# Performance work log

Measured on AMD Instinct MI355X. Metric: run time of the kernel, lower is better.

The kernel has to match this reference:

```python
import jax, jax.numpy as jnp
import numpy as np

H, C = 4, 32          # heads, out_channels
NEG_SLOPE = 0.2       # PyG GATConv default leaky-relu slope


def gat(x, edge_index, W, a_src, a_dst, b):
    """Single GATConv layer (concat heads, self-loops, no dropout).
    Returns output [N, H*C] and edge attention alpha [E+N, H]."""
    N = x.shape[0]
    h = (x @ W).reshape(N, H, C)                       # [N,H,C]
    loop = jnp.arange(N)
    src = jnp.concatenate([edge_index[0], loop])       # messages src -> dst
    dst = jnp.concatenate([edge_index[1], loop])
    a_s = jnp.sum(h * a_src, axis=-1)                  # [N,H]
    a_d = jnp.sum(h * a_dst, axis=-1)                  # [N,H]
    e = jax.nn.leaky_relu(a_s[src] + a_d[dst], NEG_SLOPE)   # [E+N,H]
    m = jax.ops.segment_max(e, dst, num_segments=N)
    p = jnp.exp(e - m[dst])
    z = jax.ops.segment_sum(p, dst, num_segments=N)
    alpha = p / z[dst]                                 # softmax per destination
    out = jax.ops.segment_sum(alpha[:, :, None] * h[src], dst, num_segments=N)
    return out.reshape(N, H * C) + b, alpha


def setup_inputs() -> dict:
    key = jax.random.key(0)
    ks = jax.random.split(key, 12)
    N, K, F_IN, E, Dg = 50000, 1000, 128, 800000, 8
    offsets = jnp.array([1, 2, 3, 5, 7, 11, 13, 17])   # circulant group graph

    x = jax.random.normal(ks[0], (N, F_IN), dtype=jnp.float32)
    edge_index = jax.random.randint(ks[1], (2, E), 0, N)
    x_g = jax.random.normal(ks[2], (K, F_IN), dtype=jnp.float32)

    src_g = jnp.repeat(jnp.arange(K), Dg)
    dst_g = (src_g + jnp.tile(offsets, K)) % K
    edge_index_g = jnp.stack([src_g, dst_g])           # [2, 8000]

    group_index = jax.random.randint(ks[3], (N,), 0, K)
    g = jnp.arange(K)[:, None]
    # symmetrized neighbor groups of each group (out- and in-neighbors), [K,16]
    nbr_idx = jnp.concatenate([(g + offsets) % K, (g - offsets) % K], axis=1)

    sc = 1.0 / np.sqrt(F_IN)
    sa = 1.0 / np.sqrt(C)
    return dict(
        x=x, edge_index=edge_index, x_g=x_g, edge_index_g=edge_index_g,
        group_index=group_index, nbr_idx=nbr_idx,
        W1=jax.random.normal(ks[4], (F_IN, H * C)) * sc,
        a_src1=jax.random.normal(ks[5], (H, C)) * sa,
        a_dst1=jax.random.normal(ks[6], (H, C)) * sa,
        b1=jnp.zeros((H * C,), jnp.float32),
        W2=jax.random.normal(ks[7], (F_IN, H * C)) * sc,
        a_src2=jax.random.normal(ks[8], (H, C)) * sa,
        a_dst2=jax.random.normal(ks[9], (H, C)) * sa,
        b2=jnp.zeros((H * C,), jnp.float32),
    )


def reference(x, edge_index, x_g, edge_index_g, group_index, nbr_idx,
              W1, a_src1, a_dst1, b1, W2, a_src2, a_dst2, b2):
    x_out, alpha1 = gat(x, edge_index, W1, a_src1, a_dst1, b1)        # [N,128]
    x_g_out, alpha2 = gat(x_g, edge_index_g, W2, a_src2, a_dst2, b2)  # [K,128]

    # per-node attention over (own group + adjacent groups in E2)
    own = x_g_out[group_index]                    # [N,F]
    cand = x_g_out[nbr_idx[group_index]]          # [N,16,F] irregular gather
    s_self = jnp.sum(x_out * own, axis=-1, keepdims=True)      # [N,1]
    s_nbr = jnp.einsum('nf,nkf->nk', x_out, cand)              # [N,16]
    w = jax.nn.softmax(jnp.concatenate([s_self, s_nbr], axis=1), axis=1)
    group_out = w[:, :1] * own + jnp.einsum('nk,nkf->nf', w[:, 1:], cand)

    x_final = x_out * 0.5 + group_out * 0.5
    return (x_final, x_g_out, alpha1, alpha2)
```

## Files before the change

kernel.cpp:

```cpp
#include <hip/hip_runtime.h>
#include <math.h>

#define NS 0.2f

__device__ __forceinline__ float lrelu(float v){ return fmaxf(v, NS * v); }
__device__ __forceinline__ float sel4(float a, float b, float c, float d, int h){
    float ab = (h & 1) ? b : a;
    float cd = (h & 1) ? d : c;
    return (h & 2) ? cd : ab;
}

__global__ __launch_bounds__(256, 4) void gemm_attn(
    const float* __restrict__ X, const float* __restrict__ W,
    const float* __restrict__ a_src, const float* __restrict__ a_dst,
    float* __restrict__ Hout, float* __restrict__ AS, float* __restrict__ AD,
    int nrows)
{
    __shared__ float Wl[64 * 128];
    int tid = threadIdx.x;
    int cg  = tid & 31;
    int rg  = tid >> 5;
    int row0 = blockIdx.x * 48 + rg * 6;

    const float* xp[6];
    int rowv[6];
    #pragma unroll
    for (int r = 0; r < 6; ++r){
        rowv[r] = row0 + r;
        int rc = min(rowv[r], nrows - 1);
        xp[r] = X + (size_t)rc * 128;
    }

    float4 acc[6] = {};
    for (int kp = 0; kp < 2; ++kp){
        __syncthreads();
        const float4* wsrc = (const float4*)(W + (size_t)kp * 64 * 128);
        for (int i = tid; i < 64 * 32; i += 256) ((float4*)Wl)[i] = wsrc[i];
        __syncthreads();
        #pragma unroll 2
        for (int k = 0; k < 64; k += 4){
            float4 xv[6];
            #pragma unroll
            for (int r = 0; r < 6; ++r)
                xv[r] = *(const float4*)(xp[r] + kp * 64 + k);
            #pragma unroll
            for (int KK = 0; KK < 4; ++KK){
                float4 wv = *(const float4*)&Wl[(k + KK) * 128 + cg * 4];
                #pragma unroll
                for (int r = 0; r < 6; ++r){
                    float xs = (KK == 0) ? xv[r].x : (KK == 1) ? xv[r].y
                             : (KK == 2) ? xv[r].z : xv[r].w;
                    acc[r].x = fmaf(xs, wv.x, acc[r].x);
                    acc[r].y = fmaf(xs, wv.y, acc[r].y);
                    acc[r].z = fmaf(xs, wv.z, acc[r].z);
                    acc[r].w = fmaf(xs, wv.w, acc[r].w);
                }
            }
        }
    }

    float4 as4 = *(const float4*)&a_src[cg * 4];
    float4 ad4 = *(const float4*)&a_dst[cg * 4];
    int head = cg >> 3;
    #pragma unroll
    for (int r = 0; r < 6; ++r){
        bool ok = rowv[r] < nrows;
        if (ok) *(float4*)&Hout[(size_t)rowv[r] * 128 + cg * 4] = acc[r];
        float s1 = acc[r].x * as4.x + acc[r].y * as4.y + acc[r].z * as4.z + acc[r].w * as4.w;
        float s2 = acc[r].x * ad4.x + acc[r].y * ad4.y + acc[r].z * ad4.z + acc[r].w * ad4.w;
        #pragma unroll
        for (int off = 1; off < 8; off <<= 1){
            s1 += __shfl_xor(s1, off);
            s2 += __shfl_xor(s2, off);
        }
        if (ok && (cg & 7) == 0){
            AS[(size_t)rowv[r] * 4 + head] = s1;
            AD[(size_t)rowv[r] * 4 + head] = s2;
        }
    }
}

__global__ void count_rank_k(
    const int* __restrict__ ei1, int E1, int N1, int* __restrict__ cnt1, int* __restrict__ rank1,
    const int* __restrict__ ei2, int E2, int N2, int* __restrict__ cnt2, int* __restrict__ rank2)
{
    int i = blockIdx.x * blockDim.x + threadIdx.x;
    int T1 = E1 + N1, T2 = E2 + N2;
    if (i < T1){
        int dst = (i < E1) ? ei1[E1 + i] : (i - E1);
        rank1[i] = atomicAdd(&cnt1[dst], 1);
    } else {
        int j = i - T1;
        if (j < T2){
            int dst = (j < E2) ? ei2[E2 + j] : (j - E2);
            rank2[j] = atomicAdd(&cnt2[dst], 1);
        }
    }
}

__global__ void fill_k(
    const int* __restrict__ ei1, int E1, int N1, const int* __restrict__ rp1,
    const int* __restrict__ rank1, int* __restrict__ cs1, int* __restrict__ ce1,
    const int* __restrict__ ei2, int E2, int N2, const int* __restrict__ rp2,
    const int* __restrict__ rank2, int* __restrict__ cs2, int* __restrict__ ce2)
{
    int i = blockIdx.x * blockDim.x + threadIdx.x;
    int T1 = E1 + N1, T2 = E2 + N2;
    if (i < T1){
        int src, dst;
        if (i < E1){ src = ei1[i]; dst = ei1[E1 + i]; } else { src = dst = i - E1; }
        int pos = rp1[dst] + rank1[i];
        cs1[pos] = src;
        ce1[pos] = i;
    } else {
        int j = i - T1;
        if (j < T2){
            int src, dst;
            if (j < E2){ src = ei2[j]; dst = ei2[E2 + j]; } else { src = dst = j - E2; }
            int pos = rp2[dst] + rank2[j];
            cs2[pos] = src;
            ce2[pos] = j;
        }
    }
}

__global__ __launch_bounds__(1024) void scan_k(
    const int* __restrict__ c1, int n1, int* __restrict__ rp1,
    const int* __restrict__ c2, int n2, int* __restrict__ rp2)
{
    const int* counts = blockIdx.x ? c2 : c1;
    int n             = blockIdx.x ? n2 : n1;
    int* row_ptr      = blockIdx.x ? rp2 : rp1;

    __shared__ int wpart[16];
    __shared__ int carry_lds;
    int tid = threadIdx.x, lane = tid & 63, wid = tid >> 6;
    if (tid == 0) carry_lds = 0;
    __syncthreads();
    for (int base = 0; base < n; base += 8192){
        int idx = base + tid * 8;
        int v[8];
        #pragma unroll
        for (int j = 0; j < 8; ++j){
            int i = idx + j;
            v[j] = (i < n) ? counts[i] : 0;
        }
        int run[8]; int tot = 0;
        #pragma unroll
        for (int j = 0; j < 8; ++j){ run[j] = tot; tot += v[j]; }
        int x = tot;
        #pragma unroll
        for (int off = 1; off < 64; off <<= 1){
            int y = __shfl_up(x, off);
            if (lane >= off) x += y;
        }
        if (lane == 63) wpart[wid] = x;
        __syncthreads();
        if (tid < 16){
            int w = wpart[tid];
            #pragma unroll
            for (int off = 1; off < 16; off <<= 1){
                int y = __shfl_up(w, off);
                if (tid >= off) w += y;
            }
            wpart[tid] = w;
        }
        __syncthreads();
        int carry = carry_lds;
        int thr_excl = carry + (wid ? wpart[wid - 1] : 0) + x - tot;
        #pragma unroll
        for (int j = 0; j < 8; ++j){
            int i = idx + j;
            if (i < n) row_ptr[i] = thr_excl + run[j];
        }
        __syncthreads();
        if (tid == 0) carry_lds += wpart[15];
        __syncthreads();
    }
    if (tid == 0) row_ptr[n] = carry_lds;
}

__global__ __launch_bounds__(256) void aggregate(
    const int* __restrict__ row_ptr, const int* __restrict__ csr_src,
    const int* __restrict__ csr_eid, const float* __restrict__ Hbuf,
    const float* __restrict__ AS, const float* __restrict__ AD,
    const float* __restrict__ bias,
    float* __restrict__ alpha_out, float* __restrict__ out, int ndst)
{
    int gw = (int)((blockIdx.x * (size_t)blockDim.x + threadIdx.x) >> 6);
    if (gw >= ndst) return;
    int lane = threadIdx.x & 63;
    int s = row_ptr[gw], e = row_ptr[gw + 1];
    const float4 ad4 = *(const float4*)&AD[(size_t)gw * 4];

    int i0 = s + lane;
    bool has = (i0 < e);
    int src0 = 0, eid0 = 0;
    float4 e4 = make_float4(-INFINITY, -INFINITY, -INFINITY, -INFINITY);
    if (has){
        src0 = csr_src[i0];
        eid0 = csr_eid[i0];
        float4 a = *(const float4*)&AS[(size_t)src0 * 4];
        e4.x = lrelu(a.x + ad4.x); e4.y = lrelu(a.y + ad4.y);
        e4.z = lrelu(a.z + ad4.z); e4.w = lrelu(a.w + ad4.w);
    }
    float m0 = e4.x, m1 = e4.y, m2 = e4.z, m3 = e4.w;
    for (int i = s + 64 + lane; i < e; i += 64){
        int src = csr_src[i];
        float4 a = *(const float4*)&AS[(size_t)src * 4];
        m0 = fmaxf(m0, lrelu(a.x + ad4.x)); m1 = fmaxf(m1, lrelu(a.y + ad4.y));
        m2 = fmaxf(m2, lrelu(a.z + ad4.z)); m3 = fmaxf(m3, lrelu(a.w + ad4.w));
    }
    #pragma unroll
    for (int off = 32; off >= 1; off >>= 1){
        m0 = fmaxf(m0, __shfl_xor(m0, off));
        m1 = fmaxf(m1, __shfl_xor(m1, off));
        m2 = fmaxf(m2, __shfl_xor(m2, off));
        m3 = fmaxf(m3, __shfl_xor(m3, off));
    }
    float4 p4 = make_float4(0.f, 0.f, 0.f, 0.f);
    if (has){
        p4.x = __expf(e4.x - m0); p4.y = __expf(e4.y - m1);
        p4.z = __expf(e4.z - m2); p4.w = __expf(e4.w - m3);
    }
    float z0 = p4.x, z1 = p4.y, z2 = p4.z, z3 = p4.w;
    for (int i = s + 64 + lane; i < e; i += 64){
        int src = csr_src[i];
        float4 a = *(const float4*)&AS[(size_t)src * 4];
        z0 += __expf(lrelu(a.x + ad4.x) - m0);
        z1 += __expf(lrelu(a.y + ad4.y) - m1);
        z2 += __expf(lrelu(a.z + ad4.z) - m2);
        z3 += __expf(lrelu(a.w + ad4.w) - m3);
    }
    #pragma unroll
    for (int off = 32; off >= 1; off >>= 1){
        z0 += __shfl_xor(z0, off);
        z1 += __shfl_xor(z1, off);
        z2 += __shfl_xor(z2, off);
        z3 += __shfl_xor(z3, off);
    }
    float4 rz = make_float4(1.f / z0, 1.f / z1, 1.f / z2, 1.f / z3);

    if (has){
        float4 al;
        al.x = p4.x * rz.x; al.y = p4.y * rz.y;
        al.z = p4.z * rz.z; al.w = p4.w * rz.w;
        *(float4*)&alpha_out[(size_t)eid0 * 4] = al;
    }
    for (int i = s + 64 + lane; i < e; i += 64){
        int src = csr_src[i]; int eid = csr_eid[i];
        float4 a = *(const float4*)&AS[(size_t)src * 4];
        float4 al;
        al.x = __expf(lrelu(a.x + ad4.x) - m0) * rz.x;
        al.y = __expf(lrelu(a.y + ad4.y) - m1) * rz.y;
        al.z = __expf(lrelu(a.z + ad4.z) - m2) * rz.z;
        al.w = __expf(lrelu(a.w + ad4.w) - m3) * rz.w;
        *(float4*)&alpha_out[(size_t)eid * 4] = al;
    }

    int sub = lane >> 5, c = lane & 31, head = c >> 3;
    float mh  = sel4(m0, m1, m2, m3, head);
    float rzh = sel4(rz.x, rz.y, rz.z, rz.w, head);
    float adh = sel4(ad4.x, ad4.y, ad4.z, ad4.w, head);
    float4 acc0 = make_float4(0.f, 0.f, 0.f, 0.f);
    float4 acc1 = make_float4(0.f, 0.f, 0.f, 0.f);
    int ne   = e - s;
    int nreg = min(ne, 64);
    int nit  = (nreg + 3) >> 2;
    for (int j = 0; j < nit; ++j){
        int idx0 = 4 * j + sub;
        int idx1 = idx0 + 2;
        bool v0 = idx0 < nreg, v1 = idx1 < nreg;
        int r0 = v0 ? idx0 : 0, r1 = v1 ? idx1 : 0;
        float ax0 = __shfl(p4.x, r0), ay0 = __shfl(p4.y, r0);
        float az0 = __shfl(p4.z, r0), aw0 = __shfl(p4.w, r0);
        int sv0 = __shfl(src0, r0);
        float ax1 = __shfl(p4.x, r1), ay1 = __shfl(p4.y, r1);
        float az1 = __shfl(p4.z, r1), aw1 = __shfl(p4.w, r1);
        int sv1 = __shfl(src0, r1);
        float ph0 = v0 ? sel4(ax0, ay0, az0, aw0, head) : 0.f;
        float ph1 = v1 ? sel4(ax1, ay1, az1, aw1, head) : 0.f;
        const float4 hv0 = *(const float4*)&Hbuf[(size_t)sv0 * 128 + c * 4];
        const float4 hv1 = *(const float4*)&Hbuf[(size_t)sv1 * 128 + c * 4];
        acc0.x = fmaf(ph0, hv0.x, acc0.x);
        acc0.y = fmaf(ph0, hv0.y, acc0.y);
        acc0.z = fmaf(ph0, hv0.z, acc0.z);
        acc0.w = fmaf(ph0, hv0.w, acc0.w);
        acc1.x = fmaf(ph1, hv1.x, acc1.x);
        acc1.y = fmaf(ph1, hv1.y, acc1.y);
        acc1.z = fmaf(ph1, hv1.z, acc1.z);
        acc1.w = fmaf(ph1, hv1.w, acc1.w);
    }
    for (int t = s + 64 + sub; t < e; t += 2){
        int srcv = csr_src[t];
        float a = AS[(size_t)srcv * 4 + head];
        float ph = __expf(lrelu(a + adh) - mh);
        const float4 hv = *(const float4*)&Hbuf[(size_t)srcv * 128 + c * 4];
        acc0.x = fmaf(ph, hv.x, acc0.x);
        acc0.y = fmaf(ph, hv.y, acc0.y);
        acc0.z = fmaf(ph, hv.z, acc0.z);
        acc0.w = fmaf(ph, hv.w, acc0.w);
    }
    float4 acc;
    acc.x = acc0.x + acc1.x;
    acc.y = acc0.y + acc1.y;
    acc.z = acc0.z + acc1.z;
    acc.w = acc0.w + acc1.w;
    acc.x += __shfl_xor(acc.x, 32);
    acc.y += __shfl_xor(acc.y, 32);
    acc.z += __shfl_xor(acc.z, 32);
    acc.w += __shfl_xor(acc.w, 32);
    if (sub == 0){
        float4 bv = *(const float4*)&bias[c * 4];
        float4 o;
        o.x = acc.x * rzh + bv.x;
        o.y = acc.y * rzh + bv.y;
        o.z = acc.z * rzh + bv.z;
        o.w = acc.w * rzh + bv.w;
        *(float4*)&out[(size_t)gw * 128 + c * 4] = o;
    }
}

__global__ __launch_bounds__(256) void mix_k(
    const int* __restrict__ group_index, const int* __restrict__ nbr_idx,
    const float* __restrict__ xg, float* __restrict__ xf, int N)
{
    int gwv = (int)((blockIdx.x * (size_t)blockDim.x + threadIdx.x) >> 6);
    int lane = threadIdx.x & 63;
    int sl = lane & 15, ns = lane >> 4;
    int gw = gwv * 4 + ns;
    bool valid = gw < N;
    int gwc = min(gw, N - 1);
    int g = group_index[gwc];
    int ch = sl * 8;

    const float* xfrow = xf + (size_t)gwc * 128 + ch;
    float4 xa = *(const float4*)xfrow;
    float4 xb = *(const float4*)(xfrow + 4);

    int ids[17];
    ids[0] = g;
    {
        const int4* nb = (const int4*)&nbr_idx[g * 16];
        int4 n0 = nb[0], n1 = nb[1], n2 = nb[2], n3 = nb[3];
        ids[1] = n0.x;  ids[2] = n0.y;  ids[3] = n0.z;  ids[4] = n0.w;
        ids[5] = n1.x;  ids[6] = n1.y;  ids[7] = n1.z;  ids[8] = n1.w;
        ids[9] = n2.x;  ids[10] = n2.y; ids[11] = n2.z; ids[12] = n2.w;
        ids[13] = n3.x; ids[14] = n3.y; ids[15] = n3.z; ids[16] = n3.w;
    }

    float dn[17];
    #pragma unroll
    for (int k = 0; k < 17; ++k){
        const float* cr = xg + (size_t)ids[k] * 128 + ch;
        float4 ca = *(const float4*)cr;
        float4 cb = *(const float4*)(cr + 4);
        float d = xa.x * ca.x + xa.y * ca.y + xa.z * ca.z + xa.w * ca.w
                + xb.x * cb.x + xb.y * cb.y + xb.z * cb.z + xb.w * cb.w;
        d += __shfl_xor(d, 1);
        d += __shfl_xor(d, 2);
        d += __shfl_xor(d, 4);
        d += __shfl_xor(d, 8);
        dn[k] = d;
    }

    float mx = dn[0];
    #pragma unroll
    for (int k = 1; k < 17; ++k) mx = fmaxf(mx, dn[k]);
    float w[17]; float sum = 0.f;
    #pragma unroll
    for (int k = 0; k < 17; ++k){ w[k] = __expf(dn[k] - mx); sum += w[k]; }
    float inv = 1.0f / sum;

    float4 aa = make_float4(0.f, 0.f, 0.f, 0.f);
    float4 ab = make_float4(0.f, 0.f, 0.f, 0.f);
    #pragma unroll
    for (int k = 0; k < 17; ++k){
        const float* cr = xg + (size_t)ids[k] * 128 + ch;
        float4 ca = *(const float4*)cr;
        float4 cb = *(const float4*)(cr + 4);
        aa.x = fmaf(w[k], ca.x, aa.x); aa.y = fmaf(w[k], ca.y, aa.y);
        aa.z = fmaf(w[k], ca.z, aa.z); aa.w = fmaf(w[k], ca.w, aa.w);
        ab.x = fmaf(w[k], cb.x, ab.x); ab.y = fmaf(w[k], cb.y, ab.y);
        ab.z = fmaf(w[k], cb.z, ab.z); ab.w = fmaf(w[k], cb.w, ab.w);
    }

    if (valid){
        float* orow = xf + (size_t)gw * 128 + ch;
        float4 r0, r1;
        r0.x = 0.5f * xa.x + 0.5f * aa.x * inv;
        r0.y = 0.5f * xa.y + 0.5f * aa.y * inv;
        r0.z = 0.5f * xa.z + 0.5f * aa.z * inv;
        r0.w = 0.5f * xa.w + 0.5f * aa.w * inv;
        r1.x = 0.5f * xb.x + 0.5f * ab.x * inv;
        r1.y = 0.5f * xb.y + 0.5f * ab.y * inv;
        r1.z = 0.5f * xb.z + 0.5f * ab.z * inv;
        r1.w = 0.5f * xb.w + 0.5f * ab.w * inv;
        *(float4*)orow = r0;
        *(float4*)(orow + 4) = r1;
    }
}

extern "C" void kernel_launch(void* const* d_in, const int* in_sizes, int n_in,
                              void* d_out, int out_size, void* d_ws, size_t ws_size,
                              hipStream_t stream)
{
    const float* x    = (const float*)d_in[0];
    const int*   ei   = (const int*)  d_in[1];
    const float* xg   = (const float*)d_in[2];
    const int*   eig  = (const int*)  d_in[3];
    const int*   gidx = (const int*)  d_in[4];
    const int*   nbr  = (const int*)  d_in[5];
    const float* W1   = (const float*)d_in[6];
    const float* as1w = (const float*)d_in[7];
    const float* ad1w = (const float*)d_in[8];
    const float* b1   = (const float*)d_in[9];
    const float* W2   = (const float*)d_in[10];
    const float* as2w = (const float*)d_in[11];
    const float* ad2w = (const float*)d_in[12];
    const float* b2   = (const float*)d_in[13];

    const int N  = in_sizes[0] / 128;
    const int E  = in_sizes[1] / 2;
    const int K  = in_sizes[2] / 128;
    const int Eg = in_sizes[3] / 2;
    const int ET1 = E + N;
    const int ET2 = Eg + K;

    float* h1  = (float*)d_ws;
    float* h2  = h1 + (size_t)N * 128;
    float* as1 = h2 + (size_t)K * 128;
    float* ad1 = as1 + (size_t)N * 4;
    float* as2 = ad1 + (size_t)N * 4;
    float* ad2 = as2 + (size_t)K * 4;
    int* row_ptr1 = (int*)(ad2 + (size_t)K * 4);
    int* row_ptr2 = row_ptr1 + (N + 1);
    int* cnt1     = row_ptr2 + (K + 1);
    int* cnt2     = cnt1 + N;
    int* csr_src1 = cnt2 + K;
    int* csr_eid1 = csr_src1 + ET1;
    int* csr_src2 = csr_eid1 + ET1;
    int* csr_eid2 = csr_src2 + ET2;

    float* xfinal = (float*)d_out;
    float* xgout  = xfinal + (size_t)N * 128;
    float* alpha1 = xgout + (size_t)K * 128;
    float* alpha2 = alpha1 + (size_t)ET1 * 4;

    int* rank1 = (int*)alpha1;
    int* rank2 = (int*)alpha2;

    hipMemsetAsync(cnt1, 0, (size_t)(N + K) * sizeof(int), stream);

    int TT = ET1 + ET2;
    count_rank_k<<<(TT + 255) / 256, 256, 0, stream>>>(
        ei, E, N, cnt1, rank1, eig, Eg, K, cnt2, rank2);

    scan_k<<<2, 1024, 0, stream>>>(cnt1, N, row_ptr1, cnt2, K, row_ptr2);

    fill_k<<<(TT + 255) / 256, 256, 0, stream>>>(
        ei, E, N, row_ptr1, rank1, csr_src1, csr_eid1,
        eig, Eg, K, row_ptr2, rank2, csr_src2, csr_eid2);

    gemm_attn<<<(N + 47) / 48, 256, 0, stream>>>(x,  W1, as1w, ad1w, h1, as1, ad1, N);
    gemm_attn<<<(K + 47) / 48, 256, 0, stream>>>(xg, W2, as2w, ad2w, h2, as2, ad2, K);

    aggregate<<<(int)(((size_t)N * 64 + 255) / 256), 256, 0, stream>>>(
        row_ptr1, csr_src1, csr_eid1, h1, as1, ad1, b1, alpha1, xfinal, N);
    aggregate<<<(int)(((size_t)K * 64 + 255) / 256), 256, 0, stream>>>(
        row_ptr2, csr_src2, csr_eid2, h2, as2, ad2, b2, alpha2, xgout, K);

    mix_k<<<(int)(((size_t)N * 16 + 255) / 256), 256, 0, stream>>>(gidx, nbr, xgout, xfinal, N);
}
```

Measured before the change: 399.8 us.

## Store projected features in fp16 and fuse group mixing into node aggregation

The projected feature buffer H is now stored as half precision, which halves the bytes moved by the irregular per-edge gathers in aggregate. The group graph is computed first, and the final group-attention mix is folded into the node aggregate kernel's epilogue. This removes the separate mix_k pass that re-read and re-wrote the N x 128 output. The aggregate loop is simplified to recompute exp per edge instead of reusing register-cached probabilities via shuffles. This adds exp work and fp16 rounding error in the aggregated outputs.

```diff
diff --git a/kernel.cpp b/kernel.cpp
--- a/kernel.cpp
+++ b/kernel.cpp
@@ -1,5 +1,7 @@
 #include <hip/hip_runtime.h>
+#include <hip/hip_fp16.h>
 #include <math.h>
+#include <string.h>
 
 #define NS 0.2f
 
@@ -13,7 +15,7 @@
 __global__ __launch_bounds__(256, 4) void gemm_attn(
     const float* __restrict__ X, const float* __restrict__ W,
     const float* __restrict__ a_src, const float* __restrict__ a_dst,
-    float* __restrict__ Hout, float* __restrict__ AS, float* __restrict__ AD,
+    __half* __restrict__ Hout, float* __restrict__ AS, float* __restrict__ AD,
     int nrows)
 {
     __shared__ float Wl[64 * 128];
@@ -65,7 +67,13 @@
     #pragma unroll
     for (int r = 0; r < 6; ++r){
         bool ok = rowv[r] < nrows;
-        if (ok) *(float4*)&Hout[(size_t)rowv[r] * 128 + cg * 4] = acc[r];
+        if (ok){
+            __half2 p01 = __floats2half2_rn(acc[r].x, acc[r].y);
+            __half2 p23 = __floats2half2_rn(acc[r].z, acc[r].w);
+            __half2* hp = (__half2*)(Hout + (size_t)rowv[r] * 128 + cg * 4);
+            hp[0] = p01;
+            hp[1] = p23;
+        }
         float s1 = acc[r].x * as4.x + acc[r].y * as4.y + acc[r].z * as4.z + acc[r].w * as4.w;
         float s2 = acc[r].x * ad4.x + acc[r].y * ad4.y + acc[r].z * ad4.z + acc[r].w * ad4.w;
         #pragma unroll
@@ -180,12 +188,15 @@
     if (tid == 0) row_ptr[n] = carry_lds;
 }
 
+template<int GROUP>
 __global__ __launch_bounds__(256) void aggregate(
     const int* __restrict__ row_ptr, const int* __restrict__ csr_src,
-    const int* __restrict__ csr_eid, const float* __restrict__ Hbuf,
+    const int* __restrict__ csr_eid, const __half* __restrict__ Hbuf,
     const float* __restrict__ AS, const float* __restrict__ AD,
     const float* __restrict__ bias,
-    float* __restrict__ alpha_out, float* __restrict__ out, int ndst)
+    float* __restrict__ alpha_out, float* __restrict__ out, int ndst,
+    const int* __restrict__ group_index, const int* __restrict__ nbr_idx,
+    const float* __restrict__ xg)
 {
     int gw = (int)((blockIdx.x * (size_t)blockDim.x + threadIdx.x) >> 6);
     if (gw >= ndst) return;
@@ -262,142 +273,93 @@
     float mh  = sel4(m0, m1, m2, m3, head);
     float rzh = sel4(rz.x, rz.y, rz.z, rz.w, head);
     float adh = sel4(ad4.x, ad4.y, ad4.z, ad4.w, head);
-    float4 acc0 = make_float4(0.f, 0.f, 0.f, 0.f);
-    float4 acc1 = make_float4(0.f, 0.f, 0.f, 0.f);
-    int ne   = e - s;
-    int nreg = min(ne, 64);
-    int nit  = (nreg + 3) >> 2;
-    for (int j = 0; j < nit; ++j){
-        int idx0 = 4 * j + sub;
-        int idx1 = idx0 + 2;
-        bool v0 = idx0 < nreg, v1 = idx1 < nreg;
-        int r0 = v0 ? idx0 : 0, r1 = v1 ? idx1 : 0;
-        float ax0 = __shfl(p4.x, r0), ay0 = __shfl(p4.y, r0);
-        float az0 = __shfl(p4.z, r0), aw0 = __shfl(p4.w, r0);
-        int sv0 = __shfl(src0, r0);
-        float ax1 = __shfl(p4.x, r1), ay1 = __shfl(p4.y, r1);
-        float az1 = __shfl(p4.z, r1), aw1 = __shfl(p4.w, r1);
-        int sv1 = __shfl(src0, r1);
-        float ph0 = v0 ? sel4(ax0, ay0, az0, aw0, head) : 0.f;
-        float ph1 = v1 ? sel4(ax1, ay1, az1, aw1, head) : 0.f;
-        const float4 hv0 = *(const float4*)&Hbuf[(size_t)sv0 * 128 + c * 4];
-        const float4 hv1 = *(const float4*)&Hbuf[(size_t)sv1 * 128 + c * 4];
-        acc0.x = fmaf(ph0, hv0.x, acc0.x);
-        acc0.y = fmaf(ph0, hv0.y, acc0.y);
-        acc0.z = fmaf(ph0, hv0.z, acc0.z);
-        acc0.w = fmaf(ph0, hv0.w, acc0.w);
-        acc1.x = fmaf(ph1, hv1.x, acc1.x);
-        acc1.y = fmaf(ph1, hv1.y, acc1.y);
-        acc1.z = fmaf(ph1, hv1.z, acc1.z);
-        acc1.w = fmaf(ph1, hv1.w, acc1.w);
-    }
-    for (int t = s + 64 + sub; t < e; t += 2){
-        int srcv = csr_src[t];
-        float a = AS[(size_t)srcv * 4 + head];
-        float ph = __expf(lrelu(a + adh) - mh);
-        const float4 hv = *(const float4*)&Hbuf[(size_t)srcv * 128 + c * 4];
-        acc0.x = fmaf(ph, hv.x, acc0.x);
-        acc0.y = fmaf(ph, hv.y, acc0.y);
-        acc0.z = fmaf(ph, hv.z, acc0.z);
-        acc0.w = fmaf(ph, hv.w, acc0.w);
-    }
-    float4 acc;
-    acc.x = acc0.x + acc1.x;
-    acc.y = acc0.y + acc1.y;
-    acc.z = acc0.z + acc1.z;
-    acc.w = acc0.w + acc1.w;
+    float4 acc = make_float4(0.f, 0.f, 0.f, 0.f);
+    for (int t0 = s + sub; t0 < e; t0 += 4){
+        int t1 = t0 + 2;
+        bool v1 = t1 < e;
+        int u1 = v1 ? t1 : t0;
+        int sv0 = csr_src[t0];
+        int sv1 = csr_src[u1];
+        float a0 = AS[(size_t)sv0 * 4 + head];
+        float a1 = AS[(size_t)sv1 * 4 + head];
+        uint2 r0 = *(const uint2*)(Hbuf + (size_t)sv0 * 128 + c * 4);
+        uint2 r1 = *(const uint2*)(Hbuf + (size_t)sv1 * 128 + c * 4);
+        float ph0 = __expf(lrelu(a0 + adh) - mh);
+        float ph1 = v1 ? __expf(lrelu(a1 + adh) - mh) : 0.f;
+        __half2 h01, h23;
+        memcpy(&h01, &r0.x, 4); memcpy(&h23, &r0.y, 4);
+        float2 f01 = __half22float2(h01), f23 = __half22float2(h23);
+        acc.x = fmaf(ph0, f01.x, acc.x);
+        acc.y = fmaf(ph0, f01.y, acc.y);
+        acc.z = fmaf(ph0, f23.x, acc.z);
+        acc.w = fmaf(ph0, f23.y, acc.w);
+        memcpy(&h01, &r1.x, 4); memcpy(&h23, &r1.y, 4);
+        f01 = __half22float2(h01); f23 = __half22float2(h23);
+        acc.x = fmaf(ph1, f01.x, acc.x);
+        acc.y = fmaf(ph1, f01.y, acc.y);
+        acc.z = fmaf(ph1, f23.x, acc.z);
+        acc.w = fmaf(ph1, f23.y, acc.w);
+    }
     acc.x += __shfl_xor(acc.x, 32);
     acc.y += __shfl_xor(acc.y, 32);
     acc.z += __shfl_xor(acc.z, 32);
     acc.w += __shfl_xor(acc.w, 32);
+
+    float4 bv = *(const float4*)&bias[c * 4];
+    float4 o;
+    o.x = acc.x * rzh + bv.x;
+    o.y = acc.y * rzh + bv.y;
+    o.z = acc.z * rzh + bv.z;
+    o.w = acc.w * rzh + bv.w;
+
+    if (GROUP == 0){
+        if (sub == 0)
+            *(float4*)&out[(size_t)gw * 128 + c * 4] = o;
+        return;
+    }
+
     if (sub == 0){
-        float4 bv = *(const float4*)&bias[c * 4];
-        float4 o;
-        o.x = acc.x * rzh + bv.x;
-        o.y = acc.y * rzh + bv.y;
-        o.z = acc.z * rzh + bv.z;
-        o.w = acc.w * rzh + bv.w;
-        *(float4*)&out[(size_t)gw * 128 + c * 4] = o;
-    }
-}
-
-__global__ __launch_bounds__(256) void mix_k(
-    const int* __restrict__ group_index, const int* __restrict__ nbr_idx,
-    const float* __restrict__ xg, float* __restrict__ xf, int N)
-{
-    int gwv = (int)((blockIdx.x * (size_t)blockDim.x + threadIdx.x) >> 6);
-    int lane = threadIdx.x & 63;
-    int sl = lane & 15, ns = lane >> 4;
-    int gw = gwv * 4 + ns;
-    bool valid = gw < N;
-    int gwc = min(gw, N - 1);
-    int g = group_index[gwc];
-    int ch = sl * 8;
-
-    const float* xfrow = xf + (size_t)gwc * 128 + ch;
-    float4 xa = *(const float4*)xfrow;
-    float4 xb = *(const float4*)(xfrow + 4);
-
-    int ids[17];
-    ids[0] = g;
-    {
-        const int4* nb = (const int4*)&nbr_idx[g * 16];
-        int4 n0 = nb[0], n1 = nb[1], n2 = nb[2], n3 = nb[3];
-        ids[1] = n0.x;  ids[2] = n0.y;  ids[3] = n0.z;  ids[4] = n0.w;
-        ids[5] = n1.x;  ids[6] = n1.y;  ids[7] = n1.z;  ids[8] = n1.w;
-        ids[9] = n2.x;  ids[10] = n2.y; ids[11] = n2.z; ids[12] = n2.w;
-        ids[13] = n3.x; ids[14] = n3.y; ids[15] = n3.z; ids[16] = n3.w;
-    }
-
-    float dn[17];
-    #pragma unroll
-    for (int k = 0; k < 17; ++k){
-        const float* cr = xg + (size_t)ids[k] * 128 + ch;
-        float4 ca = *(const float4*)cr;
-        float4 cb = *(const float4*)(cr + 4);
-        float d = xa.x * ca.x + xa.y * ca.y + xa.z * ca.z + xa.w * ca.w
-                + xb.x * cb.x + xb.y * cb.y + xb.z * cb.z + xb.w * cb.w;
-        d += __shfl_xor(d, 1);
-        d += __shfl_xor(d, 2);
-        d += __shfl_xor(d, 4);
-        d += __shfl_xor(d, 8);
-        dn[k] = d;
-    }
-
-    float mx = dn[0];
-    #pragma unroll
-    for (int k = 1; k < 17; ++k) mx = fmaxf(mx, dn[k]);
-    float w[17]; float sum = 0.f;
-    #pragma unroll
-    for (int k = 0; k < 17; ++k){ w[k] = __expf(dn[k] - mx); sum += w[k]; }
-    float inv = 1.0f / sum;
-
-    float4 aa = make_float4(0.f, 0.f, 0.f, 0.f);
-    float4 ab = make_float4(0.f, 0.f, 0.f, 0.f);
-    #pragma unroll
-    for (int k = 0; k < 17; ++k){
-        const float* cr = xg + (size_t)ids[k] * 128 + ch;
-        float4 ca = *(const float4*)cr;
-        float4 cb = *(const float4*)(cr + 4);
-        aa.x = fmaf(w[k], ca.x, aa.x); aa.y = fmaf(w[k], ca.y, aa.y);
-        aa.z = fmaf(w[k], ca.z, aa.z); aa.w = fmaf(w[k], ca.w, aa.w);
-        ab.x = fmaf(w[k], cb.x, ab.x); ab.y = fmaf(w[k], cb.y, ab.y);
-        ab.z = fmaf(w[k], cb.z, ab.z); ab.w = fmaf(w[k], cb.w, ab.w);
-    }
-
-    if (valid){
-        float* orow = xf + (size_t)gw * 128 + ch;
-        float4 r0, r1;
-        r0.x = 0.5f * xa.x + 0.5f * aa.x * inv;
-        r0.y = 0.5f * xa.y + 0.5f * aa.y * inv;
-        r0.z = 0.5f * xa.z + 0.5f * aa.z * inv;
-        r0.w = 0.5f * xa.w + 0.5f * aa.w * inv;
-        r1.x = 0.5f * xb.x + 0.5f * ab.x * inv;
-        r1.y = 0.5f * xb.y + 0.5f * ab.y * inv;
-        r1.z = 0.5f * xb.z + 0.5f * ab.z * inv;
-        r1.w = 0.5f * xb.w + 0.5f * ab.w * inv;
-        *(float4*)orow = r0;
-        *(float4*)(orow + 4) = r1;
+        int g = group_index[gw];
+        int ids[17];
+        ids[0] = g;
+        #pragma unroll
+        for (int k = 0; k < 16; ++k) ids[k + 1] = nbr_idx[g * 16 + k];
+
+        float dn[17];
+        #pragma unroll
+        for (int k = 0; k < 17; ++k){
+            const float4 cv = *(const float4*)&xg[(size_t)ids[k] * 128 + c * 4];
+            float d = o.x * cv.x + o.y * cv.y + o.z * cv.z + o.w * cv.w;
+            d += __shfl_xor(d, 1);
+            d += __shfl_xor(d, 2);
+            d += __shfl_xor(d, 4);
+            d += __shfl_xor(d, 8);
+            d += __shfl_xor(d, 16);
+            dn[k] = d;
+        }
+        float mx = dn[0];
+        #pragma unroll
+        for (int k = 1; k < 17; ++k) mx = fmaxf(mx, dn[k]);
+        float wgt[17]; float sum = 0.f;
+        #pragma unroll
+        for (int k = 0; k < 17; ++k){ wgt[k] = __expf(dn[k] - mx); sum += wgt[k]; }
+        float inv = 1.0f / sum;
+
+        float4 ga = make_float4(0.f, 0.f, 0.f, 0.f);
+        #pragma unroll
+        for (int k = 0; k < 17; ++k){
+            const float4 cv = *(const float4*)&xg[(size_t)ids[k] * 128 + c * 4];
+            ga.x = fmaf(wgt[k], cv.x, ga.x);
+            ga.y = fmaf(wgt[k], cv.y, ga.y);
+            ga.z = fmaf(wgt[k], cv.z, ga.z);
+            ga.w = fmaf(wgt[k], cv.w, ga.w);
+        }
+        float4 r;
+        r.x = 0.5f * o.x + 0.5f * ga.x * inv;
+        r.y = 0.5f * o.y + 0.5f * ga.y * inv;
+        r.z = 0.5f * o.z + 0.5f * ga.z * inv;
+        r.w = 0.5f * o.w + 0.5f * ga.w * inv;
+        *(float4*)&out[(size_t)gw * 128 + c * 4] = r;
     }
 }
 
@@ -427,12 +389,12 @@
     const int ET1 = E + N;
     const int ET2 = Eg + K;
 
-    float* h1  = (float*)d_ws;
-    float* h2  = h1 + (size_t)N * 128;
-    float* as1 = h2 + (size_t)K * 128;
-    float* ad1 = as1 + (size_t)N * 4;
-    float* as2 = ad1 + (size_t)N * 4;
-    float* ad2 = as2 + (size_t)K * 4;
+    __half* h1 = (__half*)d_ws;
+    __half* h2 = h1 + (size_t)N * 128;
+    float*  as1 = (float*)(h2 + (size_t)K * 128);
+    float*  ad1 = as1 + (size_t)N * 4;
+    float*  as2 = ad1 + (size_t)N * 4;
+    float*  ad2 = as2 + (size_t)K * 4;
     int* row_ptr1 = (int*)(ad2 + (size_t)K * 4);
     int* row_ptr2 = row_ptr1 + (N + 1);
     int* cnt1     = row_ptr2 + (K + 1);
@@ -462,13 +424,13 @@
         ei, E, N, row_ptr1, rank1, csr_src1, csr_eid1,
         eig, Eg, K, row_ptr2, rank2, csr_src2, csr_eid2);
 
-    gemm_attn<<<(N + 47) / 48, 256, 0, stream>>>(x,  W1, as1w, ad1w, h1, as1, ad1, N);
     gemm_attn<<<(K + 47) / 48, 256, 0, stream>>>(xg, W2, as2w, ad2w, h2, as2, ad2, K);
-
-    aggregate<<<(int)(((size_t)N * 64 + 255) / 256), 256, 0, stream>>>(
-        row_ptr1, csr_src1, csr_eid1, h1, as1, ad1, b1, alpha1, xfinal, N);
-    aggregate<<<(int)(((size_t)K * 64 + 255) / 256), 256, 0, stream>>>(
-        row_ptr2, csr_src2, csr_eid2, h2, as2, ad2, b2, alpha2, xgout, K);
-
-    mix_k<<<(int)(((size_t)N * 16 + 255) / 256), 256, 0, stream>>>(gidx, nbr, xgout, xfinal, N);
-}
+    aggregate<0><<<(int)(((size_t)K * 64 + 255) / 256), 256, 0, stream>>>(
+        row_ptr2, csr_src2, csr_eid2, h2, as2, ad2, b2, alpha2, xgout, K,
+        nullptr, nullptr, nullptr);
+
+    gemm_attn<<<(N + 47) / 48, 256, 0, stream>>>(x, W1, as1w, ad1w, h1, as1, ad1, N);
+    aggregate<1><<<(int)(((size_t)N * 64 + 255) / 256), 256, 0, stream>>>(
+        row_ptr1, csr_src1, csr_eid1, h1, as1, ad1, b1, alpha1, xfinal, N,
+        gidx, nbr, xgout);
+}
```

New measurement: 439.4 us. +9.9%, slower.

## Store projected features in fp16 and compute alpha in a separate edge-order pass

Applied to the files above, without the earlier changes.

The projected node features h are now written as fp16, which halves the bytes moved by the random-gather aggregation loop. The CSR edge-id array is removed. Aggregate now writes per-destination max and sum, and a new edge-ordered kernel recomputes alpha with coalesced writes instead of scattered ones. The scan also handles 16 elements per thread and the launches are reordered. This adds fp16 rounding error to the output and recomputes the attention logits in the extra pass.

```diff
diff --git a/kernel.cpp b/kernel.cpp
--- a/kernel.cpp
+++ b/kernel.cpp
@@ -1,5 +1,7 @@
 #include <hip/hip_runtime.h>
+#include <hip/hip_fp16.h>
 #include <math.h>
+#include <string.h>
 
 #define NS 0.2f
 
@@ -13,7 +15,7 @@
 __global__ __launch_bounds__(256, 4) void gemm_attn(
     const float* __restrict__ X, const float* __restrict__ W,
     const float* __restrict__ a_src, const float* __restrict__ a_dst,
-    float* __restrict__ Hout, float* __restrict__ AS, float* __restrict__ AD,
+    __half* __restrict__ Hout, float* __restrict__ AS, float* __restrict__ AD,
     int nrows)
 {
     __shared__ float Wl[64 * 128];
@@ -65,7 +67,13 @@
     #pragma unroll
     for (int r = 0; r < 6; ++r){
         bool ok = rowv[r] < nrows;
-        if (ok) *(float4*)&Hout[(size_t)rowv[r] * 128 + cg * 4] = acc[r];
+        if (ok){
+            __half2 p01 = __floats2half2_rn(acc[r].x, acc[r].y);
+            __half2 p23 = __floats2half2_rn(acc[r].z, acc[r].w);
+            __half2* hp = (__half2*)(Hout + (size_t)rowv[r] * 128 + cg * 4);
+            hp[0] = p01;
+            hp[1] = p23;
+        }
         float s1 = acc[r].x * as4.x + acc[r].y * as4.y + acc[r].z * as4.z + acc[r].w * as4.w;
         float s2 = acc[r].x * ad4.x + acc[r].y * ad4.y + acc[r].z * ad4.z + acc[r].w * ad4.w;
         #pragma unroll
@@ -100,26 +108,22 @@
 
 __global__ void fill_k(
     const int* __restrict__ ei1, int E1, int N1, const int* __restrict__ rp1,
-    const int* __restrict__ rank1, int* __restrict__ cs1, int* __restrict__ ce1,
+    const int* __restrict__ rank1, int* __restrict__ cs1,
     const int* __restrict__ ei2, int E2, int N2, const int* __restrict__ rp2,
-    const int* __restrict__ rank2, int* __restrict__ cs2, int* __restrict__ ce2)
+    const int* __restrict__ rank2, int* __restrict__ cs2)
 {
     int i = blockIdx.x * blockDim.x + threadIdx.x;
     int T1 = E1 + N1, T2 = E2 + N2;
     if (i < T1){
         int src, dst;
         if (i < E1){ src = ei1[i]; dst = ei1[E1 + i]; } else { src = dst = i - E1; }
-        int pos = rp1[dst] + rank1[i];
-        cs1[pos] = src;
-        ce1[pos] = i;
+        cs1[rp1[dst] + rank1[i]] = src;
     } else {
         int j = i - T1;
         if (j < T2){
             int src, dst;
             if (j < E2){ src = ei2[j]; dst = ei2[E2 + j]; } else { src = dst = j - E2; }
-            int pos = rp2[dst] + rank2[j];
-            cs2[pos] = src;
-            ce2[pos] = j;
+            cs2[rp2[dst] + rank2[j]] = src;
         }
     }
 }
@@ -137,17 +141,17 @@
     int tid = threadIdx.x, lane = tid & 63, wid = tid >> 6;
     if (tid == 0) carry_lds = 0;
     __syncthreads();
-    for (int base = 0; base < n; base += 8192){
-        int idx = base + tid * 8;
-        int v[8];
+    for (int base = 0; base < n; base += 16384){
+        int idx = base + tid * 16;
+        int v[16];
         #pragma unroll
-        for (int j = 0; j < 8; ++j){
+        for (int j = 0; j < 16; ++j){
             int i = idx + j;
             v[j] = (i < n) ? counts[i] : 0;
         }
-        int run[8]; int tot = 0;
+        int run[16]; int tot = 0;
         #pragma unroll
-        for (int j = 0; j < 8; ++j){ run[j] = tot; tot += v[j]; }
+        for (int j = 0; j < 16; ++j){ run[j] = tot; tot += v[j]; }
         int x = tot;
         #pragma unroll
         for (int off = 1; off < 64; off <<= 1){
@@ -169,7 +173,7 @@
         int carry = carry_lds;
         int thr_excl = carry + (wid ? wpart[wid - 1] : 0) + x - tot;
         #pragma unroll
-        for (int j = 0; j < 8; ++j){
+        for (int j = 0; j < 16; ++j){
             int i = idx + j;
             if (i < n) row_ptr[i] = thr_excl + run[j];
         }
@@ -182,10 +186,11 @@
 
 __global__ __launch_bounds__(256) void aggregate(
     const int* __restrict__ row_ptr, const int* __restrict__ csr_src,
-    const int* __restrict__ csr_eid, const float* __restrict__ Hbuf,
+    const __half* __restrict__ Hbuf,
     const float* __restrict__ AS, const float* __restrict__ AD,
     const float* __restrict__ bias,
-    float* __restrict__ alpha_out, float* __restrict__ out, int ndst)
+    float* __restrict__ M4, float* __restrict__ Z4,
+    float* __restrict__ out, int ndst)
 {
     int gw = (int)((blockIdx.x * (size_t)blockDim.x + threadIdx.x) >> 6);
     if (gw >= ndst) return;
@@ -195,11 +200,10 @@
 
     int i0 = s + lane;
     bool has = (i0 < e);
-    int src0 = 0, eid0 = 0;
+    int src0 = 0;
     float4 e4 = make_float4(-INFINITY, -INFINITY, -INFINITY, -INFINITY);
     if (has){
         src0 = csr_src[i0];
-        eid0 = csr_eid[i0];
         float4 a = *(const float4*)&AS[(size_t)src0 * 4];
         e4.x = lrelu(a.x + ad4.x); e4.y = lrelu(a.y + ad4.y);
         e4.z = lrelu(a.z + ad4.z); e4.w = lrelu(a.w + ad4.w);
@@ -241,21 +245,9 @@
     }
     float4 rz = make_float4(1.f / z0, 1.f / z1, 1.f / z2, 1.f / z3);
 
-    if (has){
-        float4 al;
-        al.x = p4.x * rz.x; al.y = p4.y * rz.y;
-        al.z = p4.z * rz.z; al.w = p4.w * rz.w;
-        *(float4*)&alpha_out[(size_t)eid0 * 4] = al;
-    }
-    for (int i = s + 64 + lane; i < e; i += 64){
-        int src = csr_src[i]; int eid = csr_eid[i];
-        float4 a = *(const float4*)&AS[(size_t)src * 4];
-        float4 al;
-        al.x = __expf(lrelu(a.x + ad4.x) - m0) * rz.x;
-        al.y = __expf(lrelu(a.y + ad4.y) - m1) * rz.y;
-        al.z = __expf(lrelu(a.z + ad4.z) - m2) * rz.z;
-        al.w = __expf(lrelu(a.w + ad4.w) - m3) * rz.w;
-        *(float4*)&alpha_out[(size_t)eid * 4] = al;
+    if (lane == 0){
+        *(float4*)&M4[(size_t)gw * 4] = make_float4(m0, m1, m2, m3);
+        *(float4*)&Z4[(size_t)gw * 4] = make_float4(z0, z1, z2, z3);
     }
 
     int sub = lane >> 5, c = lane & 31, head = c >> 3;
@@ -280,26 +272,34 @@
         int sv1 = __shfl(src0, r1);
         float ph0 = v0 ? sel4(ax0, ay0, az0, aw0, head) : 0.f;
         float ph1 = v1 ? sel4(ax1, ay1, az1, aw1, head) : 0.f;
-        const float4 hv0 = *(const float4*)&Hbuf[(size_t)sv0 * 128 + c * 4];
-        const float4 hv1 = *(const float4*)&Hbuf[(size_t)sv1 * 128 + c * 4];
-        acc0.x = fmaf(ph0, hv0.x, acc0.x);
-        acc0.y = fmaf(ph0, hv0.y, acc0.y);
-        acc0.z = fmaf(ph0, hv0.z, acc0.z);
-        acc0.w = fmaf(ph0, hv0.w, acc0.w);
-        acc1.x = fmaf(ph1, hv1.x, acc1.x);
-        acc1.y = fmaf(ph1, hv1.y, acc1.y);
-        acc1.z = fmaf(ph1, hv1.z, acc1.z);
-        acc1.w = fmaf(ph1, hv1.w, acc1.w);
+        uint2 g0 = *(const uint2*)(Hbuf + (size_t)sv0 * 128 + c * 4);
+        uint2 g1 = *(const uint2*)(Hbuf + (size_t)sv1 * 128 + c * 4);
+        __half2 h01, h23;
+        memcpy(&h01, &g0.x, 4); memcpy(&h23, &g0.y, 4);
+        float2 f01 = __half22float2(h01), f23 = __half22float2(h23);
+        acc0.x = fmaf(ph0, f01.x, acc0.x);
+        acc0.y = fmaf(ph0, f01.y, acc0.y);
+        acc0.z = fmaf(ph0, f23.x, acc0.z);
+        acc0.w = fmaf(ph0, f23.y, acc0.w);
+        memcpy(&h01, &g1.x, 4); memcpy(&h23, &g1.y, 4);
+        f01 = __half22float2(h01); f23 = __half22float2(h23);
+        acc1.x = fmaf(ph1, f01.x, acc1.x);
+        acc1.y = fmaf(ph1, f01.y, acc1.y);
+        acc1.z = fmaf(ph1, f23.x, acc1.z);
+        acc1.w = fmaf(ph1, f23.y, acc1.w);
     }
     for (int t = s + 64 + sub; t < e; t += 2){
         int srcv = csr_src[t];
         float a = AS[(size_t)srcv * 4 + head];
         float ph = __expf(lrelu(a + adh) - mh);
-        const float4 hv = *(const float4*)&Hbuf[(size_t)srcv * 128 + c * 4];
-        acc0.x = fmaf(ph, hv.x, acc0.x);
-        acc0.y = fmaf(ph, hv.y, acc0.y);
-        acc0.z = fmaf(ph, hv.z, acc0.z);
-        acc0.w = fmaf(ph, hv.w, acc0.w);
+        uint2 g0 = *(const uint2*)(Hbuf + (size_t)srcv * 128 + c * 4);
+        __half2 h01, h23;
+        memcpy(&h01, &g0.x, 4); memcpy(&h23, &g0.y, 4);
+        float2 f01 = __half22float2(h01), f23 = __half22float2(h23);
+        acc0.x = fmaf(ph, f01.x, acc0.x);
+        acc0.y = fmaf(ph, f01.y, acc0.y);
+        acc0.z = fmaf(ph, f23.x, acc0.z);
+        acc0.w = fmaf(ph, f23.y, acc0.w);
     }
     float4 acc;
     acc.x = acc0.x + acc1.x;
@@ -321,6 +321,41 @@
     }
 }
 
+__global__ void alpha_k(
+    const int* __restrict__ ei1, int E1, int N1,
+    const float* __restrict__ AS1, const float* __restrict__ AD1,
+    const float* __restrict__ M1, const float* __restrict__ Z1,
+    float* __restrict__ alpha1,
+    const int* __restrict__ ei2, int E2, int N2,
+    const float* __restrict__ AS2, const float* __restrict__ AD2,
+    const float* __restrict__ M2, const float* __restrict__ Z2,
+    float* __restrict__ alpha2)
+{
+    int i = blockIdx.x * blockDim.x + threadIdx.x;
+    int T1 = E1 + N1, T2 = E2 + N2;
+    const int* ei; const float *AS, *AD, *M, *Z; float* alpha;
+    int src, dst, idx;
+    if (i < T1){
+        idx = i; ei = ei1; AS = AS1; AD = AD1; M = M1; Z = Z1; alpha = alpha1;
+        if (i < E1){ src = ei[i]; dst = ei[E1 + i]; } else { src = dst = i - E1; }
+    } else {
+        int j = i - T1;
+        if (j >= T2) return;
+        idx = j; AS = AS2; AD = AD2; M = M2; Z = Z2; alpha = alpha2;
+        if (j < E2){ src = ei2[j]; dst = ei2[E2 + j]; } else { src = dst = j - E2; }
+    }
+    float4 a = *(const float4*)&AS[(size_t)src * 4];
+    float4 d = *(const float4*)&AD[(size_t)dst * 4];
+    float4 m = *(const float4*)&M[(size_t)dst * 4];
+    float4 z = *(const float4*)&Z[(size_t)dst * 4];
+    float4 al;
+    al.x = __expf(lrelu(a.x + d.x) - m.x) / z.x;
+    al.y = __expf(lrelu(a.y + d.y) - m.y) / z.y;
+    al.z = __expf(lrelu(a.z + d.z) - m.z) / z.z;
+    al.w = __expf(lrelu(a.w + d.w) - m.w) / z.w;
+    *(float4*)&alpha[(size_t)idx * 4] = al;
+}
+
 __global__ __launch_bounds__(256) void mix_k(
     const int* __restrict__ group_index, const int* __restrict__ nbr_idx,
     const float* __restrict__ xg, float* __restrict__ xf, int N)
@@ -427,20 +462,22 @@
     const int ET1 = E + N;
     const int ET2 = Eg + K;
 
-    float* h1  = (float*)d_ws;
-    float* h2  = h1 + (size_t)N * 128;
-    float* as1 = h2 + (size_t)K * 128;
-    float* ad1 = as1 + (size_t)N * 4;
-    float* as2 = ad1 + (size_t)N * 4;
-    float* ad2 = as2 + (size_t)K * 4;
-    int* row_ptr1 = (int*)(ad2 + (size_t)K * 4);
+    __half* h1 = (__half*)d_ws;
+    __half* h2 = h1 + (size_t)N * 128;
+    float*  as1 = (float*)(h2 + (size_t)K * 128);
+    float*  ad1 = as1 + (size_t)N * 4;
+    float*  as2 = ad1 + (size_t)N * 4;
+    float*  ad2 = as2 + (size_t)K * 4;
+    float*  m1  = ad2 + (size_t)K * 4;
+    float*  z1  = m1 + (size_t)N * 4;
+    float*  m2  = z1 + (size_t)N * 4;
+    float*  z2  = m2 + (size_t)K * 4;
+    int* row_ptr1 = (int*)(z2 + (size_t)K * 4);
     int* row_ptr2 = row_ptr1 + (N + 1);
     int* cnt1     = row_ptr2 + (K + 1);
     int* cnt2     = cnt1 + N;
     int* csr_src1 = cnt2 + K;
-    int* csr_eid1 = csr_src1 + ET1;
-    int* csr_src2 = csr_eid1 + ET1;
-    int* csr_eid2 = csr_src2 + ET2;
+    int* csr_src2 = csr_src1 + ET1;
 
     float* xfinal = (float*)d_out;
     float* xgout  = xfinal + (size_t)N * 128;
@@ -459,16 +496,20 @@
     scan_k<<<2, 1024, 0, stream>>>(cnt1, N, row_ptr1, cnt2, K, row_ptr2);
 
     fill_k<<<(TT + 255) / 256, 256, 0, stream>>>(
-        ei, E, N, row_ptr1, rank1, csr_src1, csr_eid1,
-        eig, Eg, K, row_ptr2, rank2, csr_src2, csr_eid2);
-
-    gemm_attn<<<(N + 47) / 48, 256, 0, stream>>>(x,  W1, as1w, ad1w, h1, as1, ad1, N);
+        ei, E, N, row_ptr1, rank1, csr_src1,
+        eig, Eg, K, row_ptr2, rank2, csr_src2);
+
     gemm_attn<<<(K + 47) / 48, 256, 0, stream>>>(xg, W2, as2w, ad2w, h2, as2, ad2, K);
-
+    aggregate<<<(int)(((size_t)K * 64 + 255) / 256), 256, 0, stream>>>(
+        row_ptr2, csr_src2, h2, as2, ad2, b2, m2, z2, xgout, K);
+
+    gemm_attn<<<(N + 47) / 48, 256, 0, stream>>>(x, W1, as1w, ad1w, h1, as1, ad1, N);
     aggregate<<<(int)(((size_t)N * 64 + 255) / 256), 256, 0, stream>>>(
-        row_ptr1, csr_src1, csr_eid1, h1, as1, ad1, b1, alpha1, xfinal, N);
-    aggregate<<<(int)(((size_t)K * 64 + 255) / 256), 256, 0, stream>>>(
-        row_ptr2, csr_src2, csr_eid2, h2, as2, ad2, b2, alpha2, xgout, K);
+        row_ptr1, csr_src1, h1, as1, ad1, b1, m1, z1, xfinal, N);
+
+    alpha_k<<<(TT + 255) / 256, 256, 0, stream>>>(
+        ei, E, N, as1, ad1, m1, z1, alpha1,
+        eig, Eg, K, as2, ad2, m2, z2, alpha2);
 
     mix_k<<<(int)(((size_t)N * 16 + 255) / 256), 256, 0, stream>>>(gidx, nbr, xgout, xfinal, N);
 }
```

Measured after the change: 386.6 us. -3.3%, faster.
